# Kernel optimization log

Measured on AMD Instinct MI355X. Metric: run time of the kernel, lower is better.

## Reference

```python
import jax, jax.numpy as jnp
import numpy as np

NUM_CLASSES = 1000
EMB_DIM = 768
BATCH = 16384
EPS = 1e-8  # torch F.cosine_similarity eps


def setup_inputs() -> dict:
    key = jax.random.key(0)
    k1, k2, k3, k4 = jax.random.split(key, 4)
    embeddings = jax.random.normal(k1, (BATCH, EMB_DIM), dtype=jnp.float32)
    logits = jax.random.normal(k2, (BATCH, NUM_CLASSES), dtype=jnp.float32)
    targets = jax.random.randint(k3, (BATCH,), 0, NUM_CLASSES, dtype=jnp.int64 if jax.config.jax_enable_x64 else jnp.int32)
    centroids = jax.random.normal(k4, (NUM_CLASSES, EMB_DIM), dtype=jnp.float32)
    u = jnp.ones((1,), dtype=jnp.float32)
    return {"embeddings": embeddings, "logits": logits, "targets": targets,
            "centroids": centroids, "u": u}


def _cosine_sim(embeddings, centroids):
    # torch cosine_similarity: x / max(||x||, eps); formulated as normalize + GEMM
    en = embeddings / jnp.maximum(jnp.linalg.norm(embeddings, axis=1, keepdims=True), EPS)
    cn = centroids / jnp.maximum(jnp.linalg.norm(centroids, axis=1, keepdims=True), EPS)
    return jnp.einsum('nd,cd->nc', en, cn)  # [N, C]


def reference(embeddings, logits, targets, centroids, u):
    n_classes = centroids.shape[0]
    # cross entropy (mean reduction)
    logp = jax.nn.log_softmax(logits, axis=1)
    ce_loss = -jnp.mean(jnp.take_along_axis(logp, targets[:, None], axis=1))

    sim = _cosine_sim(embeddings, centroids)            # [N, C]
    soft_labels = jax.nn.softmax(sim, axis=1)           # [N, C]

    hard_one_hot = jax.nn.one_hot(targets, n_classes, dtype=jnp.float32)
    similarity_to_target = jnp.sum(soft_labels * hard_one_hot, axis=1)  # [N]
    discount = 1.0 - similarity_to_target
    reg_term = jnp.mean(discount) * u                   # shape (1,)

    # mse_loss(hard_one_hot, soft_labels.detach()) -- soft_labels detached
    dist_reg = jnp.mean((hard_one_hot - jax.lax.stop_gradient(soft_labels)) ** 2)

    return ce_loss + dist_reg + reg_term                # shape (1,)
```

## Files before the change

### kernel.cpp

```cpp
#include <hip/hip_runtime.h>
#include <hip/hip_bf16.h>
#include <stdint.h>

#define BATCH 16384
#define NCLS 1000
#define NPAD 1024
#define EMB 768
#define KT 12
#define BM 128
#define BN 256
#define ABYTES 8192
#define BUFB 24576
#define GEMM_BLKS 512

typedef __attribute__((ext_vector_type(4))) float f32x4;
typedef long v2i64 __attribute__((ext_vector_type(2)));

#define GLOAD16(g, l) __builtin_amdgcn_global_load_lds(              \
    (const __attribute__((address_space(1))) unsigned int*)(g),       \
    (__attribute__((address_space(3))) unsigned int*)(l), 16, 0, 0)

__device__ __forceinline__ float d4(float4 v) {
    return v.x*v.x + v.y*v.y + v.z*v.z + v.w*v.w;
}
__device__ __forceinline__ float e4(float4 v) {
    return __expf(v.x) + __expf(v.y) + __expf(v.z) + __expf(v.w);
}
__device__ __forceinline__ unsigned int pk8(float4 v, float s) {
    int p = 0;
    p = __builtin_amdgcn_cvt_pk_fp8_f32(v.x * s, v.y * s, p, false);
    p = __builtin_amdgcn_cvt_pk_fp8_f32(v.z * s, v.w * s, p, true);
    return (unsigned int)p;
}

__global__ __launch_bounds__(256) void prep_row(
    const float* __restrict__ emb, const float* __restrict__ cent,
    const float* __restrict__ logits, const int* __restrict__ targets,
    unsigned int* __restrict__ en8, unsigned int* __restrict__ cn8,
    float* __restrict__ ce_row)
{
    __shared__ float ssp[4], esp[4], xts;
    const int b    = blockIdx.x;
    const int tid  = threadIdx.x;
    const int w    = tid >> 6;
    const int lane = tid & 63;

    if (b < BATCH) {
        const float4* er = (const float4*)(emb + (size_t)b * EMB);
        const float4* lr = (const float4*)(logits + (size_t)b * NCLS);
        const bool he = tid < 192;
        const bool hl = tid < 250;
        float4 ev = he ? er[tid] : make_float4(0.f, 0.f, 0.f, 0.f);
        float4 lv = hl ? lr[tid] : make_float4(0.f, 0.f, 0.f, 0.f);
        if (tid == 254) {
            const int t = targets[b];
            xts = logits[(size_t)b * NCLS + t];
        }
        float ss = d4(ev);
        float es = hl ? e4(lv) : 0.f;
        #pragma unroll
        for (int m = 1; m < 64; m <<= 1) {
            ss += __shfl_xor(ss, m, 64);
            es += __shfl_xor(es, m, 64);
        }
        if (lane == 0) { ssp[w] = ss; esp[w] = es; }
        __syncthreads();
        const float sstot = ssp[0] + ssp[1] + ssp[2] + ssp[3];
        const float sc = 1.0f / fmaxf(sqrtf(sstot), 1e-8f);
        if (he) en8[(size_t)b * (EMB / 4) + tid] = pk8(ev, sc);
        if (tid == 0) {
            const float estot = esp[0] + esp[1] + esp[2] + esp[3];
            ce_row[b] = __logf(estot) - xts;
        }
        return;
    }

    const int row = b - BATCH;
    const bool hv = row < NCLS;
    const bool he = tid < 192 && hv;
    const float4* cr = (const float4*)(cent + (size_t)row * EMB);
    float4 cv = he ? cr[tid] : make_float4(0.f, 0.f, 0.f, 0.f);
    float ss = d4(cv);
    #pragma unroll
    for (int m = 1; m < 64; m <<= 1) ss += __shfl_xor(ss, m, 64);
    if (lane == 0) ssp[w] = ss;
    __syncthreads();
    const float sstot = ssp[0] + ssp[1] + ssp[2] + ssp[3];
    const float sc = hv ? (1.0f / fmaxf(sqrtf(sstot), 1e-8f)) : 0.0f;
    if (tid < 192) cn8[(size_t)row * (EMB / 4) + tid] = he ? pk8(cv, sc) : 0u;
}

__global__ __launch_bounds__(256, 2) void gemm_kernel(
    const uint8_t* __restrict__ en8, const uint8_t* __restrict__ cn8,
    const int* __restrict__ targets,
    float* __restrict__ partZ, float* __restrict__ partS2,
    float* __restrict__ et_out)
{
    __shared__ __align__(128) uint8_t lds[2][BUFB];

    const int bid  = blockIdx.x;
    const int tid  = threadIdx.x;
    const int lane = tid & 63;
    const int warp = tid >> 6;

    const int g   = bid & 7;
    const int s   = bid >> 3;
    const int mb  = g * 16 + (s >> 2);
    const int nb  = s & 3;
    const int R0  = mb * BM;
    const int Nc0 = nb * BN;
    const int wr  = warp >> 1;
    const int wc  = warp & 1;
    const int l15 = lane & 15;
    const int rq  = lane >> 4;

    const int csw  = ((tid & 3) * 16) ^ (((tid >> 3) & 3) << 4);
    const int srow = tid >> 2;
    size_t asrc[2], bsrc[4];
    #pragma unroll
    for (int j = 0; j < 2; ++j) asrc[j] = (size_t)(R0  + j * 64 + srow) * EMB + csw;
    #pragma unroll
    for (int j = 0; j < 4; ++j) bsrc[j] = (size_t)(Nc0 + j * 64 + srow) * EMB + csw;
    const uint8_t* enb = en8;
    const uint8_t* cnb = cn8;

#define STAGE(b, kt) do { const size_t ko = (size_t)(kt) * 64;               \
    _Pragma("unroll") for (int j = 0; j < 2; ++j)                            \
        GLOAD16(enb + asrc[j] + ko, &lds[b][j * 4096 + tid * 16]);           \
    _Pragma("unroll") for (int j = 0; j < 4; ++j)                            \
        GLOAD16(cnb + bsrc[j] + ko, &lds[b][ABYTES + j * 4096 + tid * 16]);  \
} while (0)

    const int cx   = (rq * 16) ^ (((l15 >> 1) & 3) << 4);
    const int aoff = (wr * 64 + l15) * 64 + cx;
    const int boff = ABYTES + (wc * 128 + l15) * 64 + cx;

    f32x4 acc[4][8];
    #pragma unroll
    for (int m = 0; m < 4; ++m)
        #pragma unroll
        for (int n = 0; n < 8; ++n) acc[m][n] = (f32x4){0.f, 0.f, 0.f, 0.f};

    STAGE(0, 0);
    __syncthreads();

    for (int kt = 0; kt < KT; ++kt) {
        const int buf = kt & 1;
        if (kt + 1 < KT) STAGE(buf ^ 1, kt + 1);
        const uint8_t* L = &lds[buf][0];
        v2i64 af[4], bf[8];
        #pragma unroll
        for (int m = 0; m < 4; ++m) af[m] = *(const v2i64*)(L + aoff + m * 1024);
        #pragma unroll
        for (int n = 0; n < 8; ++n) bf[n] = *(const v2i64*)(L + boff + n * 1024);
        #pragma unroll
        for (int kk = 0; kk < 2; ++kk)
            #pragma unroll
            for (int m = 0; m < 4; ++m)
                #pragma unroll
                for (int n = 0; n < 8; ++n)
                    acc[m][n] = __builtin_amdgcn_mfma_f32_16x16x32_fp8_fp8(
                        bf[n][kk], af[m][kk], acc[m][n], 0, 0, 0);
        __syncthreads();
    }
#undef STAGE

    const int plane = nb * 2 + wc;
    #pragma unroll
    for (int m = 0; m < 4; ++m) {
        const int row = R0 + wr * 64 + m * 16 + l15;
        const int t   = targets[row];
        float z = 0.f, s2 = 0.f;
        #pragma unroll
        for (int n = 0; n < 8; ++n) {
            const int cb = Nc0 + wc * 128 + n * 16 + rq * 4;
            #pragma unroll
            for (int r = 0; r < 4; ++r) {
                const bool valid = (cb + r) < NCLS;
                float e = valid ? __expf(acc[m][n][r]) : 0.f;
                z += e; s2 += e * e;
                if (cb + r == t) et_out[row] = e;
            }
        }
        z  += __shfl_xor(z, 16, 64);  z  += __shfl_xor(z, 32, 64);
        s2 += __shfl_xor(s2, 16, 64); s2 += __shfl_xor(s2, 32, 64);
        if (rq == 0) {
            partZ [(size_t)plane * BATCH + row] = z;
            partS2[(size_t)plane * BATCH + row] = s2;
        }
    }
}

__global__ __launch_bounds__(256) void finalize1(
    const float* __restrict__ partZ, const float* __restrict__ partS2,
    const float* __restrict__ et_out, const float* __restrict__ ce_row,
    const float* __restrict__ u, float* __restrict__ fpart)
{
    __shared__ float red[4];
    const int row  = blockIdx.x * 256 + threadIdx.x;
    const int lane = threadIdx.x & 63;
    float z = 0.f, s2 = 0.f;
    #pragma unroll
    for (int i = 0; i < 8; ++i) {
        z  += partZ [(size_t)i * BATCH + row];
        s2 += partS2[(size_t)i * BATCH + row];
    }
    float et = et_out[row];
    float invz = 1.0f / z;
    float pt = et * invz;
    float c = (s2 * invz * invz - 2.0f * pt + 1.0f) * (1.0f / ((float)BATCH * (float)NCLS))
            + (1.0f - pt) * u[0] * (1.0f / (float)BATCH)
            + ce_row[row] * (1.0f / (float)BATCH);
    #pragma unroll
    for (int m = 1; m < 64; m <<= 1) c += __shfl_xor(c, m, 64);
    if (lane == 0) red[threadIdx.x >> 6] = c;
    __syncthreads();
    if (threadIdx.x == 0) fpart[blockIdx.x] = red[0] + red[1] + red[2] + red[3];
}

__global__ __launch_bounds__(64) void finalize2(
    const float* __restrict__ fpart, float* __restrict__ out)
{
    const int lane = threadIdx.x;
    float s = fpart[lane];
    #pragma unroll
    for (int m = 1; m < 64; m <<= 1) s += __shfl_xor(s, m, 64);
    if (lane == 0) out[0] = s;
}

extern "C" void kernel_launch(void* const* d_in, const int* in_sizes, int n_in,
                              void* d_out, int out_size, void* d_ws, size_t ws_size,
                              hipStream_t stream) {
    const float* emb       = (const float*)d_in[0];
    const float* logits    = (const float*)d_in[1];
    const int*   targets   = (const int*)d_in[2];
    const float* centroids = (const float*)d_in[3];
    const float* u         = (const float*)d_in[4];
    float* out = (float*)d_out;

    uint8_t* en8  = (uint8_t*)d_ws;
    uint8_t* cn8  = en8 + (size_t)BATCH * EMB;
    float* partZ  = (float*)(cn8 + (size_t)NPAD * EMB);
    float* partS2 = partZ + 8 * BATCH;
    float* et_out = partS2 + 8 * BATCH;
    float* ce_row = et_out + BATCH;
    float* fpart  = ce_row + BATCH;

    prep_row<<<BATCH + NPAD, 256, 0, stream>>>(emb, centroids, logits, targets,
                                               (unsigned int*)en8, (unsigned int*)cn8, ce_row);
    gemm_kernel<<<GEMM_BLKS, 256, 0, stream>>>(en8, cn8, targets, partZ, partS2, et_out);
    finalize1<<<BATCH / 256, 256, 0, stream>>>(partZ, partS2, et_out, ce_row, u, fpart);
    finalize2<<<1, 64, 0, stream>>>(fpart, out);
}
```

Baseline: 50.68 us.

## Make prep kernel persistent per 32 rows with double-buffered async LDS loads

```diff
diff --git a/kernel.cpp b/kernel.cpp
--- a/kernel.cpp
+++ b/kernel.cpp
@@ -13,6 +13,13 @@
 #define BUFB 24576
 #define GEMM_BLKS 512
 
+#define PREP_BATCH_BLKS 512
+#define PREP_CENT_BLKS  32
+#define PG 8
+#define EMB_B 3072
+#define LOG_B 4096
+#define PBUF (4 * EMB_B + 4 * LOG_B)
+
 typedef __attribute__((ext_vector_type(4))) float f32x4;
 typedef long v2i64 __attribute__((ext_vector_type(2)));
 
@@ -39,55 +46,83 @@
     unsigned int* __restrict__ en8, unsigned int* __restrict__ cn8,
     float* __restrict__ ce_row)
 {
-    __shared__ float ssp[4], esp[4], xts;
+    __shared__ __align__(128) uint8_t lds[2][PBUF];
     const int b    = blockIdx.x;
     const int tid  = threadIdx.x;
     const int w    = tid >> 6;
     const int lane = tid & 63;
-
-    if (b < BATCH) {
-        const float4* er = (const float4*)(emb + (size_t)b * EMB);
-        const float4* lr = (const float4*)(logits + (size_t)b * NCLS);
-        const bool he = tid < 192;
-        const bool hl = tid < 250;
-        float4 ev = he ? er[tid] : make_float4(0.f, 0.f, 0.f, 0.f);
-        float4 lv = hl ? lr[tid] : make_float4(0.f, 0.f, 0.f, 0.f);
-        if (tid == 254) {
-            const int t = targets[b];
-            xts = logits[(size_t)b * NCLS + t];
+    const bool isCent = b >= PREP_BATCH_BLKS;
+    const int rbase = isCent ? (b - PREP_BATCH_BLKS) * 32 : b * 32;
+
+#define PSTAGE(bf, g) do {                                                    \
+    const int row_ = rbase + (g) * 4 + w;                                     \
+    if (!isCent) {                                                            \
+        const uint8_t* es_ = (const uint8_t*)(emb + (size_t)row_ * EMB);      \
+        const uint8_t* ls_ = (const uint8_t*)(logits + (size_t)row_ * NCLS);  \
+        _Pragma("unroll") for (int j = 0; j < 3; ++j)                         \
+            GLOAD16(es_ + (lane + j * 64) * 16,                               \
+                    &lds[bf][w * EMB_B + j * 1024 + lane * 16]);              \
+        _Pragma("unroll") for (int j = 0; j < 3; ++j)                         \
+            GLOAD16(ls_ + (lane + j * 64) * 16,                               \
+                    &lds[bf][4 * EMB_B + w * LOG_B + j * 1024 + lane * 16]);  \
+        if (lane < 58)                                                        \
+            GLOAD16(ls_ + (lane + 192) * 16,                                  \
+                    &lds[bf][4 * EMB_B + w * LOG_B + 3072 + lane * 16]);      \
+    } else {                                                                  \
+        const int cr_ = (row_ < NCLS) ? row_ : NCLS - 1;                      \
+        const uint8_t* es_ = (const uint8_t*)(cent + (size_t)cr_ * EMB);      \
+        _Pragma("unroll") for (int j = 0; j < 3; ++j)                         \
+            GLOAD16(es_ + (lane + j * 64) * 16,                               \
+                    &lds[bf][w * EMB_B + j * 1024 + lane * 16]);              \
+    }                                                                         \
+} while (0)
+
+    int buf = 0;
+    PSTAGE(0, 0);
+    __syncthreads();
+
+    for (int g = 0; g < PG; ++g) {
+        if (g + 1 < PG) PSTAGE(buf ^ 1, g + 1);
+
+        const int row = rbase + g * 4 + w;
+        const uint8_t* eb = &lds[buf][w * EMB_B];
+        float4 e0 = *(const float4*)(eb + lane * 16);
+        float4 e1 = *(const float4*)(eb + 1024 + lane * 16);
+        float4 e2 = *(const float4*)(eb + 2048 + lane * 16);
+        float ss = d4(e0) + d4(e1) + d4(e2);
+        #pragma unroll
+        for (int m = 1; m < 64; m <<= 1) ss += __shfl_xor(ss, m, 64);
+
+        if (!isCent) {
+            const float sc = 1.0f / fmaxf(sqrtf(ss), 1e-8f);
+            unsigned int* op = en8 + (size_t)row * (EMB / 4) + lane;
+            op[0] = pk8(e0, sc); op[64] = pk8(e1, sc); op[128] = pk8(e2, sc);
+
+            const uint8_t* lb = &lds[buf][4 * EMB_B + w * LOG_B];
+            float4 l0 = *(const float4*)(lb + lane * 16);
+            float4 l1 = *(const float4*)(lb + 1024 + lane * 16);
+            float4 l2 = *(const float4*)(lb + 2048 + lane * 16);
+            float es = e4(l0) + e4(l1) + e4(l2);
+            if (lane < 58) {
+                float4 l3 = *(const float4*)(lb + 3072 + lane * 16);
+                es += e4(l3);
+            }
+            #pragma unroll
+            for (int m = 1; m < 64; m <<= 1) es += __shfl_xor(es, m, 64);
+            if (lane == 0) {
+                const int t = targets[row];
+                const float xt = *(const float*)(lb + t * 4);
+                ce_row[row] = __logf(es) - xt;
+            }
+        } else {
+            const float sc = (row < NCLS) ? (1.0f / fmaxf(sqrtf(ss), 1e-8f)) : 0.0f;
+            unsigned int* op = cn8 + (size_t)row * (EMB / 4) + lane;
+            op[0] = pk8(e0, sc); op[64] = pk8(e1, sc); op[128] = pk8(e2, sc);
         }
-        float ss = d4(ev);
-        float es = hl ? e4(lv) : 0.f;
-        #pragma unroll
-        for (int m = 1; m < 64; m <<= 1) {
-            ss += __shfl_xor(ss, m, 64);
-            es += __shfl_xor(es, m, 64);
-        }
-        if (lane == 0) { ssp[w] = ss; esp[w] = es; }
         __syncthreads();
-        const float sstot = ssp[0] + ssp[1] + ssp[2] + ssp[3];
-        const float sc = 1.0f / fmaxf(sqrtf(sstot), 1e-8f);
-        if (he) en8[(size_t)b * (EMB / 4) + tid] = pk8(ev, sc);
-        if (tid == 0) {
-            const float estot = esp[0] + esp[1] + esp[2] + esp[3];
-            ce_row[b] = __logf(estot) - xts;
-        }
-        return;
-    }
-
-    const int row = b - BATCH;
-    const bool hv = row < NCLS;
-    const bool he = tid < 192 && hv;
-    const float4* cr = (const float4*)(cent + (size_t)row * EMB);
-    float4 cv = he ? cr[tid] : make_float4(0.f, 0.f, 0.f, 0.f);
-    float ss = d4(cv);
-    #pragma unroll
-    for (int m = 1; m < 64; m <<= 1) ss += __shfl_xor(ss, m, 64);
-    if (lane == 0) ssp[w] = ss;
-    __syncthreads();
-    const float sstot = ssp[0] + ssp[1] + ssp[2] + ssp[3];
-    const float sc = hv ? (1.0f / fmaxf(sqrtf(sstot), 1e-8f)) : 0.0f;
-    if (tid < 192) cn8[(size_t)row * (EMB / 4) + tid] = he ? pk8(cv, sc) : 0u;
+        buf ^= 1;
+    }
+#undef PSTAGE
 }
 
 __global__ __launch_bounds__(256, 2) void gemm_kernel(
@@ -246,8 +281,9 @@
     float* ce_row = et_out + BATCH;
     float* fpart  = ce_row + BATCH;
 
-    prep_row<<<BATCH + NPAD, 256, 0, stream>>>(emb, centroids, logits, targets,
-                                               (unsigned int*)en8, (unsigned int*)cn8, ce_row);
+    prep_row<<<PREP_BATCH_BLKS + PREP_CENT_BLKS, 256, 0, stream>>>(
+        emb, centroids, logits, targets,
+        (unsigned int*)en8, (unsigned int*)cn8, ce_row);
     gemm_kernel<<<GEMM_BLKS, 256, 0, stream>>>(en8, cn8, targets, partZ, partS2, et_out);
     finalize1<<<BATCH / 256, 256, 0, stream>>>(partZ, partS2, et_out, ce_row, u, fpart);
     finalize2<<<1, 64, 0, stream>>>(fpart, out);
```

Result: slower. 56.03 us (+10.6%).

## Move cross-entropy row work into GEMM launch and halve GEMM N-tile

Applied to the files above, without the earlier changes.

```diff
diff --git a/kernel.cpp b/kernel.cpp
--- a/kernel.cpp
+++ b/kernel.cpp
@@ -8,10 +8,11 @@
 #define EMB 768
 #define KT 12
 #define BM 128
-#define BN 256
+#define BN 128
 #define ABYTES 8192
-#define BUFB 24576
-#define GEMM_BLKS 512
+#define BUFB 16384
+#define GEMM_BLKS 1024
+#define CE_BLKS 4096
 
 typedef __attribute__((ext_vector_type(4))) float f32x4;
 typedef long v2i64 __attribute__((ext_vector_type(2)));
@@ -33,68 +34,41 @@
     return (unsigned int)p;
 }
 
-__global__ __launch_bounds__(256) void prep_row(
+__global__ __launch_bounds__(192) void prep_ec(
     const float* __restrict__ emb, const float* __restrict__ cent,
-    const float* __restrict__ logits, const int* __restrict__ targets,
-    unsigned int* __restrict__ en8, unsigned int* __restrict__ cn8,
-    float* __restrict__ ce_row)
-{
-    __shared__ float ssp[4], esp[4], xts;
+    unsigned int* __restrict__ en8, unsigned int* __restrict__ cn8)
+{
+    __shared__ float ssp[3];
     const int b    = blockIdx.x;
     const int tid  = threadIdx.x;
     const int w    = tid >> 6;
     const int lane = tid & 63;
 
-    if (b < BATCH) {
-        const float4* er = (const float4*)(emb + (size_t)b * EMB);
-        const float4* lr = (const float4*)(logits + (size_t)b * NCLS);
-        const bool he = tid < 192;
-        const bool hl = tid < 250;
-        float4 ev = he ? er[tid] : make_float4(0.f, 0.f, 0.f, 0.f);
-        float4 lv = hl ? lr[tid] : make_float4(0.f, 0.f, 0.f, 0.f);
-        if (tid == 254) {
-            const int t = targets[b];
-            xts = logits[(size_t)b * NCLS + t];
-        }
-        float ss = d4(ev);
-        float es = hl ? e4(lv) : 0.f;
-        #pragma unroll
-        for (int m = 1; m < 64; m <<= 1) {
-            ss += __shfl_xor(ss, m, 64);
-            es += __shfl_xor(es, m, 64);
-        }
-        if (lane == 0) { ssp[w] = ss; esp[w] = es; }
-        __syncthreads();
-        const float sstot = ssp[0] + ssp[1] + ssp[2] + ssp[3];
-        const float sc = 1.0f / fmaxf(sqrtf(sstot), 1e-8f);
-        if (he) en8[(size_t)b * (EMB / 4) + tid] = pk8(ev, sc);
-        if (tid == 0) {
-            const float estot = esp[0] + esp[1] + esp[2] + esp[3];
-            ce_row[b] = __logf(estot) - xts;
-        }
-        return;
-    }
-
-    const int row = b - BATCH;
-    const bool hv = row < NCLS;
-    const bool he = tid < 192 && hv;
-    const float4* cr = (const float4*)(cent + (size_t)row * EMB);
-    float4 cv = he ? cr[tid] : make_float4(0.f, 0.f, 0.f, 0.f);
-    float ss = d4(cv);
+    const bool isC = b >= BATCH;
+    const int row  = isC ? b - BATCH : b;
+    const bool valid = !isC || row < NCLS;
+
+    const float4* src = isC ? (const float4*)(cent + (size_t)row * EMB)
+                            : (const float4*)(emb + (size_t)row * EMB);
+    float4 v = (valid) ? src[tid] : make_float4(0.f, 0.f, 0.f, 0.f);
+
+    float ss = d4(v);
     #pragma unroll
     for (int m = 1; m < 64; m <<= 1) ss += __shfl_xor(ss, m, 64);
     if (lane == 0) ssp[w] = ss;
     __syncthreads();
-    const float sstot = ssp[0] + ssp[1] + ssp[2] + ssp[3];
-    const float sc = hv ? (1.0f / fmaxf(sqrtf(sstot), 1e-8f)) : 0.0f;
-    if (tid < 192) cn8[(size_t)row * (EMB / 4) + tid] = he ? pk8(cv, sc) : 0u;
-}
-
-__global__ __launch_bounds__(256, 2) void gemm_kernel(
+    const float tot = ssp[0] + ssp[1] + ssp[2];
+    const float sc = valid ? (1.0f / fmaxf(sqrtf(tot), 1e-8f)) : 0.0f;
+
+    unsigned int* op = (isC ? cn8 : en8) + (size_t)row * (EMB / 4);
+    op[tid] = pk8(v, sc);
+}
+
+__global__ __launch_bounds__(256) void gemm_ce(
     const uint8_t* __restrict__ en8, const uint8_t* __restrict__ cn8,
-    const int* __restrict__ targets,
+    const float* __restrict__ logits, const int* __restrict__ targets,
     float* __restrict__ partZ, float* __restrict__ partS2,
-    float* __restrict__ et_out)
+    float* __restrict__ et_out, float* __restrict__ ce_row)
 {
     __shared__ __align__(128) uint8_t lds[2][BUFB];
 
@@ -103,10 +77,30 @@
     const int lane = tid & 63;
     const int warp = tid >> 6;
 
+    if (bid >= GEMM_BLKS) {
+        const int row = (bid - GEMM_BLKS) * 4 + warp;
+        const float* rp = logits + (size_t)row * NCLS;
+        const float4* r4 = (const float4*)rp;
+        float4 v0 = r4[lane];
+        float4 v1 = r4[lane + 64];
+        float4 v2 = r4[lane + 128];
+        const bool has = lane < 58;
+        float4 v3 = has ? r4[lane + 192] : v0;
+        float s = e4(v0) + e4(v1) + e4(v2);
+        if (has) s += e4(v3);
+        #pragma unroll
+        for (int m = 1; m < 64; m <<= 1) s += __shfl_xor(s, m, 64);
+        if (lane == 0) {
+            float xt = rp[targets[row]];
+            ce_row[row] = __logf(s) - xt;
+        }
+        return;
+    }
+
     const int g   = bid & 7;
     const int s   = bid >> 3;
-    const int mb  = g * 16 + (s >> 2);
-    const int nb  = s & 3;
+    const int mb  = g * 16 + (s >> 3);
+    const int nb  = s & 7;
     const int R0  = mb * BM;
     const int Nc0 = nb * BN;
     const int wr  = warp >> 1;
@@ -116,30 +110,31 @@
 
     const int csw  = ((tid & 3) * 16) ^ (((tid >> 3) & 3) << 4);
     const int srow = tid >> 2;
-    size_t asrc[2], bsrc[4];
-    #pragma unroll
-    for (int j = 0; j < 2; ++j) asrc[j] = (size_t)(R0  + j * 64 + srow) * EMB + csw;
-    #pragma unroll
-    for (int j = 0; j < 4; ++j) bsrc[j] = (size_t)(Nc0 + j * 64 + srow) * EMB + csw;
+    size_t asrc[2], bsrc[2];
+    #pragma unroll
+    for (int j = 0; j < 2; ++j) {
+        asrc[j] = (size_t)(R0  + j * 64 + srow) * EMB + csw;
+        bsrc[j] = (size_t)(Nc0 + j * 64 + srow) * EMB + csw;
+    }
     const uint8_t* enb = en8;
     const uint8_t* cnb = cn8;
 
 #define STAGE(b, kt) do { const size_t ko = (size_t)(kt) * 64;               \
     _Pragma("unroll") for (int j = 0; j < 2; ++j)                            \
         GLOAD16(enb + asrc[j] + ko, &lds[b][j * 4096 + tid * 16]);           \
-    _Pragma("unroll") for (int j = 0; j < 4; ++j)                            \
+    _Pragma("unroll") for (int j = 0; j < 2; ++j)                            \
         GLOAD16(cnb + bsrc[j] + ko, &lds[b][ABYTES + j * 4096 + tid * 16]);  \
 } while (0)
 
     const int cx   = (rq * 16) ^ (((l15 >> 1) & 3) << 4);
     const int aoff = (wr * 64 + l15) * 64 + cx;
-    const int boff = ABYTES + (wc * 128 + l15) * 64 + cx;
-
-    f32x4 acc[4][8];
+    const int boff = ABYTES + (wc * 64 + l15) * 64 + cx;
+
+    f32x4 acc[4][4];
     #pragma unroll
     for (int m = 0; m < 4; ++m)
         #pragma unroll
-        for (int n = 0; n < 8; ++n) acc[m][n] = (f32x4){0.f, 0.f, 0.f, 0.f};
+        for (int n = 0; n < 4; ++n) acc[m][n] = (f32x4){0.f, 0.f, 0.f, 0.f};
 
     STAGE(0, 0);
     __syncthreads();
@@ -148,17 +143,17 @@
         const int buf = kt & 1;
         if (kt + 1 < KT) STAGE(buf ^ 1, kt + 1);
         const uint8_t* L = &lds[buf][0];
-        v2i64 af[4], bf[8];
+        v2i64 af[4], bf[4];
         #pragma unroll
         for (int m = 0; m < 4; ++m) af[m] = *(const v2i64*)(L + aoff + m * 1024);
         #pragma unroll
-        for (int n = 0; n < 8; ++n) bf[n] = *(const v2i64*)(L + boff + n * 1024);
+        for (int n = 0; n < 4; ++n) bf[n] = *(const v2i64*)(L + boff + n * 1024);
         #pragma unroll
         for (int kk = 0; kk < 2; ++kk)
             #pragma unroll
             for (int m = 0; m < 4; ++m)
                 #pragma unroll
-                for (int n = 0; n < 8; ++n)
+                for (int n = 0; n < 4; ++n)
                     acc[m][n] = __builtin_amdgcn_mfma_f32_16x16x32_fp8_fp8(
                         bf[n][kk], af[m][kk], acc[m][n], 0, 0, 0);
         __syncthreads();
@@ -172,8 +167,8 @@
         const int t   = targets[row];
         float z = 0.f, s2 = 0.f;
         #pragma unroll
-        for (int n = 0; n < 8; ++n) {
-            const int cb = Nc0 + wc * 128 + n * 16 + rq * 4;
+        for (int n = 0; n < 4; ++n) {
+            const int cb = Nc0 + wc * 64 + n * 16 + rq * 4;
             #pragma unroll
             for (int r = 0; r < 4; ++r) {
                 const bool valid = (cb + r) < NCLS;
@@ -201,7 +196,7 @@
     const int lane = threadIdx.x & 63;
     float z = 0.f, s2 = 0.f;
     #pragma unroll
-    for (int i = 0; i < 8; ++i) {
+    for (int i = 0; i < 16; ++i) {
         z  += partZ [(size_t)i * BATCH + row];
         s2 += partS2[(size_t)i * BATCH + row];
     }
@@ -241,14 +236,15 @@
     uint8_t* en8  = (uint8_t*)d_ws;
     uint8_t* cn8  = en8 + (size_t)BATCH * EMB;
     float* partZ  = (float*)(cn8 + (size_t)NPAD * EMB);
-    float* partS2 = partZ + 8 * BATCH;
-    float* et_out = partS2 + 8 * BATCH;
+    float* partS2 = partZ + 16 * BATCH;
+    float* et_out = partS2 + 16 * BATCH;
     float* ce_row = et_out + BATCH;
     float* fpart  = ce_row + BATCH;
 
-    prep_row<<<BATCH + NPAD, 256, 0, stream>>>(emb, centroids, logits, targets,
-                                               (unsigned int*)en8, (unsigned int*)cn8, ce_row);
-    gemm_kernel<<<GEMM_BLKS, 256, 0, stream>>>(en8, cn8, targets, partZ, partS2, et_out);
+    prep_ec<<<BATCH + NPAD, 192, 0, stream>>>(emb, centroids,
+                                              (unsigned int*)en8, (unsigned int*)cn8);
+    gemm_ce<<<GEMM_BLKS + CE_BLKS, 256, 0, stream>>>(en8, cn8, logits, targets,
+                                                     partZ, partS2, et_out, ce_row);
     finalize1<<<BATCH / 256, 256, 0, stream>>>(partZ, partS2, et_out, ce_row, u, fpart);
     finalize2<<<1, 64, 0, stream>>>(fpart, out);
 }
```

New measurement: 49.52 us, median of 2. -2.3%, faster.

## Restructure prep kernel to process rows per warp with batched inline-asm loads

Applied to the files above, without the earlier changes.

```diff
diff --git a/kernel.cpp b/kernel.cpp
--- a/kernel.cpp
+++ b/kernel.cpp
@@ -12,6 +12,8 @@
 #define ABYTES 8192
 #define BUFB 24576
 #define GEMM_BLKS 512
+#define PREP_BATCH 512
+#define PREP_CENT 32
 
 typedef __attribute__((ext_vector_type(4))) float f32x4;
 typedef long v2i64 __attribute__((ext_vector_type(2)));
@@ -19,6 +21,10 @@
 #define GLOAD16(g, l) __builtin_amdgcn_global_load_lds(              \
     (const __attribute__((address_space(1))) unsigned int*)(g),       \
     (__attribute__((address_space(3))) unsigned int*)(l), 16, 0, 0)
+
+#define GL4(d, a) asm volatile("global_load_dwordx4 %0, %1, off" : "=v"(d) : "v"(a) : "memory")
+#define WAIT0() do { asm volatile("s_waitcnt vmcnt(0)" ::: "memory"); \
+                     __builtin_amdgcn_sched_barrier(0); } while (0)
 
 __device__ __forceinline__ float d4(float4 v) {
     return v.x*v.x + v.y*v.y + v.z*v.z + v.w*v.w;
@@ -33,61 +39,84 @@
     return (unsigned int)p;
 }
 
-__global__ __launch_bounds__(256) void prep_row(
+__global__ __launch_bounds__(256) void prep_asm(
     const float* __restrict__ emb, const float* __restrict__ cent,
     const float* __restrict__ logits, const int* __restrict__ targets,
     unsigned int* __restrict__ en8, unsigned int* __restrict__ cn8,
     float* __restrict__ ce_row)
 {
-    __shared__ float ssp[4], esp[4], xts;
     const int b    = blockIdx.x;
-    const int tid  = threadIdx.x;
-    const int w    = tid >> 6;
-    const int lane = tid & 63;
-
-    if (b < BATCH) {
-        const float4* er = (const float4*)(emb + (size_t)b * EMB);
-        const float4* lr = (const float4*)(logits + (size_t)b * NCLS);
-        const bool he = tid < 192;
-        const bool hl = tid < 250;
-        float4 ev = he ? er[tid] : make_float4(0.f, 0.f, 0.f, 0.f);
-        float4 lv = hl ? lr[tid] : make_float4(0.f, 0.f, 0.f, 0.f);
-        if (tid == 254) {
-            const int t = targets[b];
-            xts = logits[(size_t)b * NCLS + t];
-        }
-        float ss = d4(ev);
-        float es = hl ? e4(lv) : 0.f;
-        #pragma unroll
-        for (int m = 1; m < 64; m <<= 1) {
-            ss += __shfl_xor(ss, m, 64);
-            es += __shfl_xor(es, m, 64);
-        }
-        if (lane == 0) { ssp[w] = ss; esp[w] = es; }
-        __syncthreads();
-        const float sstot = ssp[0] + ssp[1] + ssp[2] + ssp[3];
-        const float sc = 1.0f / fmaxf(sqrtf(sstot), 1e-8f);
-        if (he) en8[(size_t)b * (EMB / 4) + tid] = pk8(ev, sc);
-        if (tid == 0) {
-            const float estot = esp[0] + esp[1] + esp[2] + esp[3];
-            ce_row[b] = __logf(estot) - xts;
+    const int w    = threadIdx.x >> 6;
+    const int lane = threadIdx.x & 63;
+
+    if (b < PREP_BATCH) {
+        const int rw = b * 32 + w * 8;
+        const bool has = lane < 58;
+
+        float xt[8];
+        #pragma unroll
+        for (int j = 0; j < 8; ++j)
+            xt[j] = logits[(size_t)(rw + j) * NCLS + targets[rw + j]];
+        #pragma unroll
+        for (int j = 0; j < 8; ++j) asm volatile("" : "+v"(xt[j]));
+
+        #pragma unroll
+        for (int p = 0; p < 4; ++p) {
+            const int r = rw + 2 * p;
+            const float* e0p = emb + (size_t)r * EMB;
+            const float* e1p = e0p + EMB;
+            const float* l0p = logits + (size_t)r * NCLS;
+            const float* l1p = l0p + NCLS;
+
+            float4 e0, e1, e2, e3, e4v, e5, l0, l1, l2, l3, l4, l5, l6, l7;
+            GL4(e0, e0p + lane * 4);        GL4(e1, e0p + lane * 4 + 256);
+            GL4(e2, e0p + lane * 4 + 512);
+            GL4(e3, e1p + lane * 4);        GL4(e4v, e1p + lane * 4 + 256);
+            GL4(e5, e1p + lane * 4 + 512);
+            GL4(l0, l0p + lane * 4);        GL4(l1, l0p + lane * 4 + 256);
+            GL4(l2, l0p + lane * 4 + 512);  GL4(l3, has ? (l0p + lane * 4 + 768) : l0p);
+            GL4(l4, l1p + lane * 4);        GL4(l5, l1p + lane * 4 + 256);
+            GL4(l6, l1p + lane * 4 + 512);  GL4(l7, has ? (l1p + lane * 4 + 768) : l1p);
+            WAIT0();
+
+            float ss0 = d4(e0) + d4(e1) + d4(e2);
+            float ss1 = d4(e3) + d4(e4v) + d4(e5);
+            float es0 = e4(l0) + e4(l1) + e4(l2);
+            float es1 = e4(l4) + e4(l5) + e4(l6);
+            if (has) { es0 += e4(l3); es1 += e4(l7); }
+            #pragma unroll
+            for (int m = 1; m < 64; m <<= 1) {
+                ss0 += __shfl_xor(ss0, m, 64); ss1 += __shfl_xor(ss1, m, 64);
+                es0 += __shfl_xor(es0, m, 64); es1 += __shfl_xor(es1, m, 64);
+            }
+            const float sc0 = 1.0f / fmaxf(sqrtf(ss0), 1e-8f);
+            const float sc1 = 1.0f / fmaxf(sqrtf(ss1), 1e-8f);
+            unsigned int* o = en8 + (size_t)r * 192 + lane;
+            o[0]   = pk8(e0, sc0); o[64]  = pk8(e1, sc0); o[128] = pk8(e2, sc0);
+            o[192] = pk8(e3, sc1); o[256] = pk8(e4v, sc1); o[320] = pk8(e5, sc1);
+            if (lane == 0) {
+                ce_row[r]     = __logf(es0) - xt[2 * p];
+                ce_row[r + 1] = __logf(es1) - xt[2 * p + 1];
+            }
         }
         return;
     }
 
-    const int row = b - BATCH;
-    const bool hv = row < NCLS;
-    const bool he = tid < 192 && hv;
-    const float4* cr = (const float4*)(cent + (size_t)row * EMB);
-    float4 cv = he ? cr[tid] : make_float4(0.f, 0.f, 0.f, 0.f);
-    float ss = d4(cv);
-    #pragma unroll
-    for (int m = 1; m < 64; m <<= 1) ss += __shfl_xor(ss, m, 64);
-    if (lane == 0) ssp[w] = ss;
-    __syncthreads();
-    const float sstot = ssp[0] + ssp[1] + ssp[2] + ssp[3];
-    const float sc = hv ? (1.0f / fmaxf(sqrtf(sstot), 1e-8f)) : 0.0f;
-    if (tid < 192) cn8[(size_t)row * (EMB / 4) + tid] = he ? pk8(cv, sc) : 0u;
+    const int c0 = (b - PREP_BATCH) * 32 + w * 8;
+    for (int j = 0; j < 8; ++j) {
+        const int row = c0 + j;
+        const bool hv = row < NCLS;
+        const float* cr = cent + (size_t)(hv ? row : NCLS - 1) * EMB;
+        float4 v0 = *((const float4*)cr + lane);
+        float4 v1 = *((const float4*)cr + lane + 64);
+        float4 v2 = *((const float4*)cr + lane + 128);
+        float ss = d4(v0) + d4(v1) + d4(v2);
+        #pragma unroll
+        for (int m = 1; m < 64; m <<= 1) ss += __shfl_xor(ss, m, 64);
+        const float sc = hv ? (1.0f / fmaxf(sqrtf(ss), 1e-8f)) : 0.0f;
+        unsigned int* op = cn8 + (size_t)row * 192 + lane;
+        op[0] = pk8(v0, sc); op[64] = pk8(v1, sc); op[128] = pk8(v2, sc);
+    }
 }
 
 __global__ __launch_bounds__(256, 2) void gemm_kernel(
@@ -246,8 +275,9 @@
     float* ce_row = et_out + BATCH;
     float* fpart  = ce_row + BATCH;
 
-    prep_row<<<BATCH + NPAD, 256, 0, stream>>>(emb, centroids, logits, targets,
-                                               (unsigned int*)en8, (unsigned int*)cn8, ce_row);
+    prep_asm<<<PREP_BATCH + PREP_CENT, 256, 0, stream>>>(
+        emb, centroids, logits, targets,
+        (unsigned int*)en8, (unsigned int*)cn8, ce_row);
     gemm_kernel<<<GEMM_BLKS, 256, 0, stream>>>(en8, cn8, targets, partZ, partS2, et_out);
     finalize1<<<BATCH / 256, 256, 0, stream>>>(partZ, partS2, et_out, ce_row, u, fpart);
     finalize2<<<1, 64, 0, stream>>>(fpart, out);
```

Result: slower. 52.48 us (+3.5%).
